# Kernel optimization log

Hardware: AMD Instinct MI355X
Metric: run time of the kernel (lower is better)

## Reference

```python
import jax, jax.numpy as jnp
import numpy as np

# init config (from init_kwargs)
VOXEL_SIZE = np.array([0.25, 0.25, 8.0], dtype=np.float32)
PC_RANGE = np.array([-50.0, -50.0, -5.0, 50.0, 50.0, 3.0], dtype=np.float32)
GRID_SIZE = np.round((PC_RANGE[3:] - PC_RANGE[:3]) / VOXEL_SIZE).astype(np.int64)  # [400, 400, 1]
N_BATCH = 4
N_TIME = 5
N_POINTS = 2_000_000


def setup_inputs() -> dict:
    key = jax.random.key(0)
    kb, kxy, kz, ki, kt = jax.random.split(key, 5)
    # points: [batch_id, x, y, z, intensity, time]; xy generated strictly inside
    # pc_range so the in-range mask in the original forward is all-True (identity
    # filter) -> static shapes, jit-compatible.
    b = jax.random.randint(kb, (N_POINTS, 1), 0, N_BATCH).astype(jnp.float32)
    xy = jax.random.uniform(kxy, (N_POINTS, 2), minval=-49.9, maxval=49.9)
    z = jax.random.uniform(kz, (N_POINTS, 1), minval=-5.0, maxval=3.0)
    inten = jax.random.uniform(ki, (N_POINTS, 1))
    t = jax.random.randint(kt, (N_POINTS, 1), 0, N_TIME).astype(jnp.float32)
    points = jnp.concatenate([b, xy, z, inten, t], axis=1)
    return {"points": points}


def reference(points):
    N = points.shape[0]
    vs = jnp.asarray(VOXEL_SIZE)
    pr = jnp.asarray(PC_RANGE)
    Gx, Gy = int(GRID_SIZE[0]), int(GRID_SIZE[1])

    # voxel coords; all points are in-range by construction (mask identity)
    coords_f = (points[:, 1:4] - pr[:3]) / vs          # (N, 3) float
    coords = coords_f.astype(jnp.int32)                # trunc == floor (coords >= 0)
    b_idx = points[:, 0].astype(jnp.int32)
    t_idx = points[:, -1].astype(jnp.int32)

    # scalar key preserving lexicographic order of (batch, x, y, time)
    key_ = ((b_idx * Gx + coords[:, 0]) * Gy + coords[:, 1]) * N_TIME + t_idx  # (N,)
    unq_keys, unq_inv = jnp.unique(key_, return_inverse=True, size=N, fill_value=-1)

    # scatter_mean of xyz per pillar
    sums = jax.ops.segment_sum(points[:, 1:4], unq_inv, num_segments=N)        # (N, 3)
    cnts = jax.ops.segment_sum(jnp.ones((N,), points.dtype), unq_inv, num_segments=N)
    mean = sums / jnp.maximum(cnts, 1.0)[:, None]

    f_cluster = points[:, 1:4] - mean[unq_inv]
    f_center = points[:, 1:3] - (coords[:, :2].astype(points.dtype) * vs[:2]
                                 + vs[:2] * 0.5 + pr[:2])
    features = jnp.concatenate([points[:, 1:5], f_cluster, f_center], axis=-1)  # (N, 9)

    # decode unique keys back to rows, reordered as (batch, time, y, x);
    # padded slots (key == -1) become -1 rows.
    valid = unq_keys >= 0
    k = jnp.where(valid, unq_keys, 0)
    tt = k % N_TIME
    k = k // N_TIME
    yy = k % Gy
    k = k // Gy
    xx = k % Gx
    bb = k // Gx
    unq = jnp.stack([bb, tt, yy, xx], axis=1)
    unq = jnp.where(valid[:, None], unq, -1)

    return features, unq, unq_inv, jnp.asarray(GRID_SIZE)
```

## Files before the change

### kernel.cpp

```cpp
#include <hip/hip_runtime.h>


#define NKEYS 3200000
#define GX 400
#define GY 400
#define NT 5

#define NBUCK 400
#define TILE 8000
#define RCAP 5632
#define NWORDS 128
#define MWORDS 125
#define NPADBLK 128

typedef __attribute__((ext_vector_type(4))) float vf4;
typedef unsigned long long u64;

__device__ __forceinline__ void make_rec(float b, float x, float y, float z,
                                         float t, int* bkt, u64* rec) {
    float u = (x + 50.0f) * 4.0f;
    float v = (y + 50.0f) * 4.0f;
    int cx = (int)u;
    int cy = (int)v;
    float dx = u - (float)cx;
    float dy = v - (float)cy;
    float dz = (z + 5.0f) * 0.125f;
    int key = (((int)b * GX + cx) * GY + cy) * NT + (int)t;
    u64 qdx = (u64)(unsigned int)rintf(dx * 4096.0f);
    u64 qdy = (u64)(unsigned int)rintf(dy * 4096.0f);
    u64 qdz = (u64)(unsigned int)rintf(dz * 32768.0f);
    *bkt = key / TILE;
    *rec = (u64)(unsigned int)key | (qdx << 22) | (qdy << 35) | (qdz << 48);
}

__global__ __launch_bounds__(1024) void bin_kernel(const vf4* __restrict__ pts4,
                                                   int n, int* __restrict__ gcnt,
                                                   u64* __restrict__ recs) {
    __shared__ int hist[NBUCK];
    __shared__ int gbaseS[NBUCK];
    int tid = threadIdx.x;
    if (tid < NBUCK) hist[tid] = 0;
    __syncthreads();

    int i = blockIdx.x * blockDim.x + tid;
    int p0 = i * 8;
    int bkt[8];
    u64 rec[8];
    int lrk[8];
    int nv = 0;
    if (p0 + 7 < n) {
        vf4 A[12];
#pragma unroll
        for (int q = 0; q < 12; ++q)
            A[q] = __builtin_nontemporal_load(pts4 + (size_t)12 * i + q);
#pragma unroll
        for (int m = 0; m < 4; ++m) {
            vf4 v0 = A[3 * m], v1 = A[3 * m + 1], v2 = A[3 * m + 2];
            make_rec(v0.x, v0.y, v0.z, v0.w, v1.y, &bkt[2 * m], &rec[2 * m]);
            make_rec(v1.z, v1.w, v2.x, v2.y, v2.w, &bkt[2 * m + 1], &rec[2 * m + 1]);
        }
        nv = 8;
    } else if (p0 < n) {
        const float* p = (const float*)pts4;
#pragma unroll
        for (int k = 0; k < 8; ++k) {
            int j = p0 + k;
            if (j < n) {
                make_rec(p[6 * j], p[6 * j + 1], p[6 * j + 2], p[6 * j + 3],
                         p[6 * j + 5], &bkt[k], &rec[k]);
                nv = k + 1;
            }
        }
    }
#pragma unroll
    for (int k = 0; k < 8; ++k)
        if (k < nv) lrk[k] = atomicAdd(&hist[bkt[k]], 1);
    __syncthreads();
    if (tid < NBUCK) gbaseS[tid] = atomicAdd(&gcnt[tid], hist[tid]);
    __syncthreads();
#pragma unroll
    for (int k = 0; k < 8; ++k)
        if (k < nv) {
            int idx = gbaseS[bkt[k]] + lrk[k];
            if (idx < RCAP)
                recs[(size_t)bkt[k] * RCAP + idx] = rec[k];
        }
}

__global__ __launch_bounds__(1024) void bucket_accum_kernel(
        const u64* __restrict__ recs, const int* __restrict__ gcnt,
        u64* __restrict__ pk, int* __restrict__ bcnt, u64* __restrict__ gmask) {
    __shared__ u64 tbl[TILE];
    __shared__ u64 msk[MWORDS];
    __shared__ int wrank[MWORDS];
    __shared__ int w0tot;
    int tid = threadIdx.x;
    int lane = tid & 63;
    int b = blockIdx.x;
    for (int s = tid; s < TILE; s += 1024) tbl[s] = 0;
    __syncthreads();
    int cnt = gcnt[b];
    if (cnt > RCAP) cnt = RCAP;
    const u64* rp = recs + (size_t)b * RCAP;
    int base = b * TILE;
    for (int r = tid; r < cnt; r += 1024) {
        u64 v = __builtin_nontemporal_load(rp + r);
        int slot = (int)(v & 0x3FFFFFULL) - base;
        u64 qdx = (v >> 22) & 0x1FFFULL;
        u64 qdy = (v >> 35) & 0x1FFFULL;
        u64 qdz = v >> 48;
        atomicAdd(&tbl[slot], qdx | (qdy << 18) | (qdz << 36) | (1ULL << 57));
    }
    __syncthreads();
#pragma unroll
    for (int j = 0; j < 8; ++j) {
        int s = tid + j * 1024;
        bool p = (s < TILE) && (tbl[s] != 0ULL);
        u64 bal = __ballot(p);
        int w = s >> 6;
        if (lane == 0 && w < MWORDS) msk[w] = bal;
    }
    __syncthreads();
    int pc = 0, xi = 0;
    if (tid < MWORDS) {
        pc = __popcll(msk[tid]);
        xi = pc;
#pragma unroll
        for (int off = 1; off < 64; off <<= 1) {
            int y = __shfl_up(xi, off, 64);
            if (lane >= off) xi += y;
        }
        if (tid == 63) w0tot = xi;
    }
    __syncthreads();
    if (tid < MWORDS) {
        int add = (tid >= 64) ? w0tot : 0;
        wrank[tid] = xi - pc + add;
        if (tid == MWORDS - 1) bcnt[b] = xi + add;
        gmask[(size_t)b * NWORDS + tid] = msk[tid];
    } else if (tid < NWORDS) {
        gmask[(size_t)b * NWORDS + tid] = 0ULL;
    }
    __syncthreads();
#pragma unroll
    for (int j = 0; j < 8; ++j) {
        int s = tid + j * 1024;
        if (s < TILE) {
            u64 v = tbl[s];
            u64 outv = 0ULL;
            if (v) {
                float cntf = (float)(unsigned int)(v >> 57);
                float rcp = 16383.0f / cntf;
                unsigned int sx = (unsigned int)(v & 0x3FFFFULL);
                unsigned int sy = (unsigned int)((v >> 18) & 0x3FFFFULL);
                unsigned int sz = (unsigned int)((v >> 36) & 0x1FFFFFULL);
                u64 mqx = (u64)(unsigned int)rintf((float)sx * rcp * 2.44140625e-4f);
                u64 mqy = (u64)(unsigned int)rintf((float)sy * rcp * 2.44140625e-4f);
                u64 mqz = (u64)(unsigned int)rintf((float)sz * rcp * 3.0517578125e-5f);
                int lr = wrank[s >> 6] +
                         __popcll(msk[s >> 6] & ((1ULL << (s & 63)) - 1ULL));
                outv = mqx | (mqy << 14) | (mqz << 28) | ((u64)lr << 42);
            }
            pk[base + s] = outv;
        }
    }
}

__global__ void scan_bcnt_kernel(const int* __restrict__ bcnt,
                                 int* __restrict__ gbase,
                                 float* __restrict__ gs) {
    __shared__ int wsum[8];
    int tid = threadIdx.x;
    int lane = tid & 63;
    int wv = tid >> 6;
    int v = (tid < NBUCK) ? bcnt[tid] : 0;
    int x = v;
#pragma unroll
    for (int off = 1; off < 64; off <<= 1) {
        int y = __shfl_up(x, off, 64);
        if (lane >= off) x += y;
    }
    if (lane == 63) wsum[wv] = x;
    __syncthreads();
    if (wv == 0) {
        int w = (lane < 8) ? wsum[lane] : 0;
#pragma unroll
        for (int off = 1; off < 8; off <<= 1) {
            int y = __shfl_up(w, off, 64);
            if (lane >= off) w += y;
        }
        if (lane < 8) wsum[lane] = w;
    }
    __syncthreads();
    int waveExcl = (wv == 0) ? 0 : wsum[wv - 1];
    if (tid < NBUCK) gbase[tid] = waveExcl + x - v;
    if (tid == 511) gbase[NBUCK] = waveExcl + x;
    if (tid == 0) { gs[0] = 400.0f; gs[1] = 400.0f; gs[2] = 1.0f; }
}

__device__ __forceinline__ void point_feat(float bfl, float x, float y, float z,
                                           float inten, float t,
                                           const u64* __restrict__ pk,
                                           const int* __restrict__ gbase,
                                           float* f, float* r) {
    float u = (x + 50.0f) * 4.0f;
    float v = (y + 50.0f) * 4.0f;
    int cx = (int)u;
    int cy = (int)v;
    int key = (((int)bfl * GX + cx) * GY + cy) * NT + (int)t;
    u64 m = pk[key];
    int bb = gbase[key / TILE];
    const float qs = 1.0f / 16383.0f;
    float mdx = (float)(unsigned int)(m & 0x3FFFULL) * qs;
    float mdy = (float)(unsigned int)((m >> 14) & 0x3FFFULL) * qs;
    float mdz = (float)(unsigned int)((m >> 28) & 0x3FFFULL) * qs;
    float bx = (float)cx * 0.25f - 50.0f;
    float by = (float)cy * 0.25f - 50.0f;
    f[0] = x;
    f[1] = y;
    f[2] = z;
    f[3] = inten;
    f[4] = x - (bx + mdx * 0.25f);
    f[5] = y - (by + mdy * 0.25f);
    f[6] = z - (-5.0f + mdz * 8.0f);
    f[7] = x - (bx + 0.125f);
    f[8] = y - (by + 0.125f);
    *r = (float)((unsigned int)(m >> 42) + bb);
}

__global__ void out_fused_kernel(const vf4* __restrict__ pts4, int n,
                                 const u64* __restrict__ pk,
                                 const int* __restrict__ gbase,
                                 const u64* __restrict__ gmask,
                                 float* __restrict__ feat,
                                 vf4* __restrict__ uinv4,
                                 vf4* __restrict__ unq4) {
    int bid = blockIdx.x;
    int tid = threadIdx.x;

    if (bid < NBUCK) {
        __shared__ u64 mw[NWORDS];
        __shared__ int w0tot;
        int lane = tid & 63;
        if (tid < NWORDS) mw[tid] = gmask[(size_t)bid * NWORDS + tid];
        __syncthreads();
        int pc = 0, xi = 0;
        if (tid < NWORDS) {
            pc = __popcll(mw[tid]);
            xi = pc;
#pragma unroll
            for (int off = 1; off < 64; off <<= 1) {
                int y = __shfl_up(xi, off, 64);
                if (lane >= off) xi += y;
            }
            if (tid == 63) w0tot = xi;
        }
        __syncthreads();
        if (tid < NWORDS) {
            int r = gbase[bid] + xi - pc + ((tid >= 64) ? w0tot : 0);
            u64 w = mw[tid];
            int keyb = bid * TILE + tid * 64;
            while (w) {
                int bit = __builtin_ctzll(w);
                w &= w - 1;
                int k = keyb + bit;
                int tt = k % NT;
                int k2 = k / NT;
                int yy = k2 % GY;
                int k3 = k2 / GY;
                int xx = k3 % GX;
                int bb = k3 / GX;
                vf4 row = {(float)bb, (float)tt, (float)yy, (float)xx};
                unq4[r] = row;
                ++r;
            }
        }
        return;
    }

    if (bid < NBUCK + NPADBLK) {
        int nu = gbase[NBUCK];
        vf4 neg = {-1.0f, -1.0f, -1.0f, -1.0f};
        for (int row = nu + (bid - NBUCK) * 256 + tid; row < n;
             row += NPADBLK * 256)
            unq4[row] = neg;
        return;
    }

    int i = (bid - NBUCK - NPADBLK) * 256 + tid;
    int p0 = i * 4;
    if (p0 >= n) return;
    if (p0 + 3 < n) {
        vf4 a0 = __builtin_nontemporal_load(pts4 + (size_t)6 * i + 0);
        vf4 a1 = __builtin_nontemporal_load(pts4 + (size_t)6 * i + 1);
        vf4 a2 = __builtin_nontemporal_load(pts4 + (size_t)6 * i + 2);
        vf4 a3 = __builtin_nontemporal_load(pts4 + (size_t)6 * i + 3);
        vf4 a4 = __builtin_nontemporal_load(pts4 + (size_t)6 * i + 4);
        vf4 a5 = __builtin_nontemporal_load(pts4 + (size_t)6 * i + 5);
        float f[36];
        float r[4];
        point_feat(a0.x, a0.y, a0.z, a0.w, a1.x, a1.y, pk, gbase, f + 0, r + 0);
        point_feat(a1.z, a1.w, a2.x, a2.y, a2.z, a2.w, pk, gbase, f + 9, r + 1);
        point_feat(a3.x, a3.y, a3.z, a3.w, a4.x, a4.y, pk, gbase, f + 18, r + 2);
        point_feat(a4.z, a4.w, a5.x, a5.y, a5.z, a5.w, pk, gbase, f + 27, r + 3);
        vf4* dst = (vf4*)(feat + (size_t)i * 36);
#pragma unroll
        for (int k = 0; k < 9; ++k) {
            vf4 o = {f[4 * k], f[4 * k + 1], f[4 * k + 2], f[4 * k + 3]};
            dst[k] = o;
        }
        vf4 rv = {r[0], r[1], r[2], r[3]};
        uinv4[i] = rv;
    } else {
        const float* p = (const float*)pts4;
        float* uinv = (float*)uinv4;
        for (int j = p0; j < n; ++j) {
            float f[9];
            float r;
            point_feat(p[6 * j], p[6 * j + 1], p[6 * j + 2], p[6 * j + 3],
                       p[6 * j + 4], p[6 * j + 5], pk, gbase, f, &r);
            for (int k = 0; k < 9; ++k) feat[(size_t)j * 9 + k] = f[k];
            uinv[j] = r;
        }
    }
}

extern "C" void kernel_launch(void* const* d_in, const int* in_sizes, int n_in,
                              void* d_out, int out_size, void* d_ws, size_t ws_size,
                              hipStream_t stream) {
    const float* pts = (const float*)d_in[0];
    int n = in_sizes[0] / 6;

    char* ws = (char*)d_ws;
    u64* pk = (u64*)ws;
    int* gcnt  = (int*)(ws + (size_t)NKEYS * 8);
    int* bcnt  = (int*)(ws + (size_t)NKEYS * 8 + 2048);
    int* gbase = (int*)(ws + (size_t)NKEYS * 8 + 4096);
    u64* gmask = (u64*)(ws + (size_t)NKEYS * 8 + 8192);

    float* feat = (float*)d_out;
    float* unq  = feat + (size_t)n * 9;
    float* uinv = feat + (size_t)n * 13;
    float* gs   = feat + (size_t)n * 14;

    u64* recs = (u64*)d_out;

    (void)hipMemsetAsync(gcnt, 0, NBUCK * sizeof(int), stream);

    int nb_bin = ((n + 7) / 8 + 1023) / 1024;
    bin_kernel<<<nb_bin, 1024, 0, stream>>>((const vf4*)pts, n, gcnt, recs);
    bucket_accum_kernel<<<NBUCK, 1024, 0, stream>>>(recs, gcnt, pk, bcnt, gmask);
    scan_bcnt_kernel<<<1, 512, 0, stream>>>(bcnt, gbase, gs);

    int nq = (n + 3) / 4;
    int nb_out = (nq + 255) / 256;
    out_fused_kernel<<<NBUCK + NPADBLK + nb_out, 256, 0, stream>>>(
        (const vf4*)pts, n, pk, gbase, gmask, feat, (vf4*)uinv, (vf4*)unq);
}
```

Measured before the change: 265.0 us.

## Stage binned records in LDS for coalesced bucketed scatter in bin kernel

The bin kernel now takes 4 points per thread instead of 8. Within each block it runs a prefix scan over the bucket histogram, reorders the records in shared memory by bucket, and then writes them out contiguously per bucket. This replaces the random per-record global scatter with mostly coalesced runs, aiming to cut write transaction overhead. In exchange it adds extra barriers, a block-wide scan and 32KB of LDS per block, and it launches twice as many blocks, which doubles the global atomic traffic on the counters.

```diff
diff --git a/kernel.cpp b/kernel.cpp
--- a/kernel.cpp
+++ b/kernel.cpp
@@ -12,6 +12,7 @@
 #define NWORDS 128
 #define MWORDS 125
 #define NPADBLK 128
+#define BINPTS 4096
 
 typedef __attribute__((ext_vector_type(4))) float vf4;
 typedef unsigned long long u64;
@@ -36,34 +37,40 @@
 __global__ __launch_bounds__(1024) void bin_kernel(const vf4* __restrict__ pts4,
                                                    int n, int* __restrict__ gcnt,
                                                    u64* __restrict__ recs) {
+    __shared__ u64 lrec[BINPTS];
     __shared__ int hist[NBUCK];
-    __shared__ int gbaseS[NBUCK];
+    __shared__ int pref[NBUCK];
+    __shared__ int dlt[NBUCK];
+    __shared__ int wsum[16];
+    __shared__ int sTotal;
     int tid = threadIdx.x;
+    int lane = tid & 63;
+    int wv = tid >> 6;
     if (tid < NBUCK) hist[tid] = 0;
     __syncthreads();
 
-    int i = blockIdx.x * blockDim.x + tid;
-    int p0 = i * 8;
-    int bkt[8];
-    u64 rec[8];
-    int lrk[8];
+    int i = blockIdx.x * 1024 + tid;
+    int p0 = i * 4;
+    int bkt[4];
+    u64 rec[4];
+    int lrk[4];
     int nv = 0;
-    if (p0 + 7 < n) {
-        vf4 A[12];
-#pragma unroll
-        for (int q = 0; q < 12; ++q)
-            A[q] = __builtin_nontemporal_load(pts4 + (size_t)12 * i + q);
-#pragma unroll
-        for (int m = 0; m < 4; ++m) {
-            vf4 v0 = A[3 * m], v1 = A[3 * m + 1], v2 = A[3 * m + 2];
-            make_rec(v0.x, v0.y, v0.z, v0.w, v1.y, &bkt[2 * m], &rec[2 * m]);
-            make_rec(v1.z, v1.w, v2.x, v2.y, v2.w, &bkt[2 * m + 1], &rec[2 * m + 1]);
-        }
-        nv = 8;
+    if (p0 + 3 < n) {
+        vf4 a0 = __builtin_nontemporal_load(pts4 + (size_t)6 * i + 0);
+        vf4 a1 = __builtin_nontemporal_load(pts4 + (size_t)6 * i + 1);
+        vf4 a2 = __builtin_nontemporal_load(pts4 + (size_t)6 * i + 2);
+        vf4 a3 = __builtin_nontemporal_load(pts4 + (size_t)6 * i + 3);
+        vf4 a4 = __builtin_nontemporal_load(pts4 + (size_t)6 * i + 4);
+        vf4 a5 = __builtin_nontemporal_load(pts4 + (size_t)6 * i + 5);
+        make_rec(a0.x, a0.y, a0.z, a0.w, a1.y, &bkt[0], &rec[0]);
+        make_rec(a1.z, a1.w, a2.x, a2.y, a2.w, &bkt[1], &rec[1]);
+        make_rec(a3.x, a3.y, a3.z, a3.w, a4.y, &bkt[2], &rec[2]);
+        make_rec(a4.z, a4.w, a5.x, a5.y, a5.w, &bkt[3], &rec[3]);
+        nv = 4;
     } else if (p0 < n) {
         const float* p = (const float*)pts4;
 #pragma unroll
-        for (int k = 0; k < 8; ++k) {
+        for (int k = 0; k < 4; ++k) {
             int j = p0 + k;
             if (j < n) {
                 make_rec(p[6 * j], p[6 * j + 1], p[6 * j + 2], p[6 * j + 3],
@@ -73,18 +80,57 @@
         }
     }
 #pragma unroll
-    for (int k = 0; k < 8; ++k)
+    for (int k = 0; k < 4; ++k)
         if (k < nv) lrk[k] = atomicAdd(&hist[bkt[k]], 1);
     __syncthreads();
-    if (tid < NBUCK) gbaseS[tid] = atomicAdd(&gcnt[tid], hist[tid]);
-    __syncthreads();
-#pragma unroll
-    for (int k = 0; k < 8; ++k)
-        if (k < nv) {
-            int idx = gbaseS[bkt[k]] + lrk[k];
-            if (idx < RCAP)
-                recs[(size_t)bkt[k] * RCAP + idx] = rec[k];
-        }
+
+    int v = (tid < NBUCK) ? hist[tid] : 0;
+    int x = v;
+#pragma unroll
+    for (int off = 1; off < 64; off <<= 1) {
+        int y = __shfl_up(x, off, 64);
+        if (lane >= off) x += y;
+    }
+    if (lane == 63) wsum[wv] = x;
+    __syncthreads();
+    if (wv == 0) {
+        int w = (lane < 16) ? wsum[lane] : 0;
+#pragma unroll
+        for (int off = 1; off < 16; off <<= 1) {
+            int y = __shfl_up(w, off, 64);
+            if (lane >= off) w += y;
+        }
+        if (lane < 16) wsum[lane] = w;
+    }
+    __syncthreads();
+    int waveExcl = (wv == 0) ? 0 : wsum[wv - 1];
+    int excl = waveExcl + x - v;
+    if (tid < NBUCK) {
+        pref[tid] = excl;
+        int gb = atomicAdd(&gcnt[tid], v);
+        dlt[tid] = gb - excl;
+    }
+    if (tid == 1023) sTotal = waveExcl + x;
+    __syncthreads();
+
+#pragma unroll
+    for (int k = 0; k < 4; ++k)
+        if (k < nv) lrec[pref[bkt[k]] + lrk[k]] = rec[k];
+    __syncthreads();
+
+    int tot = sTotal;
+#pragma unroll
+    for (int j = 0; j < 4; ++j) {
+        int slot = tid + j * 1024;
+        if (slot < tot) {
+            u64 rc = lrec[slot];
+            int key = (int)(rc & 0x3FFFFFULL);
+            int bk = key / TILE;
+            int gpos = dlt[bk] + slot;
+            if (gpos < RCAP)
+                recs[(size_t)bk * RCAP + gpos] = rc;
+        }
+    }
 }
 
 __global__ __launch_bounds__(1024) void bucket_accum_kernel(
@@ -347,7 +393,7 @@
 
     (void)hipMemsetAsync(gcnt, 0, NBUCK * sizeof(int), stream);
 
-    int nb_bin = ((n + 7) / 8 + 1023) / 1024;
+    int nb_bin = (n + BINPTS - 1) / BINPTS;
     bin_kernel<<<nb_bin, 1024, 0, stream>>>((const vf4*)pts, n, gcnt, recs);
     bucket_accum_kernel<<<NBUCK, 1024, 0, stream>>>(recs, gcnt, pk, bcnt, gmask);
     scan_bcnt_kernel<<<1, 512, 0, stream>>>(bcnt, gbase, gs);
```

Measured after the change: 259.3 us. 1.02x faster.
